# Performance work log

Hardware: AMD Instinct MI355X
Metric: run time of the kernel (lower is better)

Reference implementation:

```python
import jax, jax.numpy as jnp
import numpy as np

EPS = 1e-20

def efficient_squash(s):
    # Efficient-CapsNet squash: (1 - 1/e^||s||) * s/||s||
    n = jnp.linalg.norm(s, axis=-1, keepdims=True)
    return (1.0 - 1.0 / (jnp.exp(n) + EPS)) * (s / (n + EPS))

def setup_inputs() -> dict:
    key = jax.random.key(0)
    k1, k2 = jax.random.split(key)
    B, N, D_in = 32, 2048, 16
    K, D_out = 32, 16
    x = jax.random.normal(k1, (B, N, D_in), dtype=jnp.float32)
    # he_normal fan_in = N * D_in * ... ; use simple scaled normal init
    w = jax.random.normal(k2, (K, N, D_in, D_out), dtype=jnp.float32) * 0.05
    b = jnp.zeros((K, N, 1), dtype=jnp.float32)
    return {"x": x, "w": w, "b": b}

def reference(x, w, b):
    D_out = w.shape[-1]
    # projection: [B,N,D_in] x [K,N,D_in,D_out] -> [B,K,N,D_out]
    u = jnp.einsum('bji,kjiz->bkjz', x, w)
    # agreement c_{bkj} = sum_{i,z} u_{bkjz} u_{bkiz} = <u_j, sum_i u_i>
    t = jnp.sum(u, axis=2)                      # [B,K,D_out]
    c = jnp.einsum('bkjz,bkz->bkj', u, t)[..., None]  # [B,K,N,1]
    c = c / jnp.sqrt(jnp.asarray(D_out, jnp.float32))
    c = jax.nn.softmax(c, axis=1)               # softmax over capsules K
    c = c + b                                   # broadcast [K,N,1]
    s = jnp.sum(u * c, axis=2)                  # [B,K,D_out]
    return efficient_squash(s)
```

## Files before the change

### kernel.cpp

```cpp
#include <hip/hip_runtime.h>

#define NN 2048
#define KK 32

typedef __attribute__((ext_vector_type(8))) short short8;
typedef __attribute__((ext_vector_type(4))) float f32x4;

#define WS_TPART 0UL
#define WS_SPART 33554432UL
#define WS_TP2   50331648UL
#define WS_SP2   51380224UL
#define WS_T     52428800UL
#define WS_NEED  52494336UL

__device__ __forceinline__ short8 pack8(const float* r) {
    short8 o;
#pragma unroll
    for (int e = 0; e < 8; ++e)
        o[e] = (short)(unsigned short)((__float_as_uint(r[e]) + 0x8000u) >> 16);
    return o;
}
__device__ __forceinline__ short8 sel8(bool keep, short8 v) {
    union { short8 s; unsigned u[4]; } a, b;
    a.s = v;
#pragma unroll
    for (int i = 0; i < 4; ++i) b.u[i] = keep ? a.u[i] : 0u;
    return b.s;
}

__global__ __launch_bounds__(512)
void kT(const float* __restrict__ x, const float* __restrict__ w,
        float* __restrict__ t_part)
{
    const int tid = threadIdx.x;
    const int wv = tid >> 6, l = tid & 63;
    const int z = l & 15, g = l >> 4;
    const int jl = g >> 1, ih = g & 1;
    const int j0 = blockIdx.x * 4;

    f32x4 C[4][2];
#pragma unroll
    for (int ckl = 0; ckl < 4; ++ckl)
#pragma unroll
        for (int bh = 0; bh < 2; ++bh) C[ckl][bh] = (f32x4){0.f, 0.f, 0.f, 0.f};

#pragma unroll
    for (int p = 0; p < 2; ++p) {
        const int jp = j0 + p * 2 + jl;
        short8 Af[2];
#pragma unroll
        for (int bh = 0; bh < 2; ++bh) {
            const float* xp = x + ((size_t)(bh * 16 + z) * NN + jp) * 16 + ih * 8;
            float ar[8];
            float4 v0 = *reinterpret_cast<const float4*>(xp);
            float4 v1 = *reinterpret_cast<const float4*>(xp + 4);
            ar[0]=v0.x; ar[1]=v0.y; ar[2]=v0.z; ar[3]=v0.w;
            ar[4]=v1.x; ar[5]=v1.y; ar[6]=v1.z; ar[7]=v1.w;
            Af[bh] = pack8(ar);
        }
        short8 Bf[4];
#pragma unroll
        for (int ckl = 0; ckl < 4; ++ckl) {
            const int ck = wv * 4 + ckl;
            const float* wp = w + ((size_t)ck * NN + jp) * 256 + ih * 128 + z;
            float br[8];
#pragma unroll
            for (int e = 0; e < 8; ++e) br[e] = wp[e * 16];
            Bf[ckl] = pack8(br);
        }
#pragma unroll
        for (int ckl = 0; ckl < 4; ++ckl)
#pragma unroll
            for (int bh = 0; bh < 2; ++bh)
                C[ckl][bh] = __builtin_amdgcn_mfma_f32_16x16x32_bf16(
                    Af[bh], Bf[ckl], C[ckl][bh], 0, 0, 0);
    }

    float* tp = t_part + (size_t)blockIdx.x * 16384;
#pragma unroll
    for (int ckl = 0; ckl < 4; ++ckl)
#pragma unroll
        for (int bh = 0; bh < 2; ++bh)
#pragma unroll
            for (int r = 0; r < 4; ++r)
                tp[((bh * 16 + g * 4 + r) * 32 + wv * 4 + ckl) * 16 + z] =
                    C[ckl][bh][r];
}

__global__ __launch_bounds__(256)
void kred32(const float* __restrict__ src, float* __restrict__ dst)
{
    const int idx = blockIdx.x * 256 + threadIdx.x;
    const int c4 = idx & 4095, ch = idx >> 12;
    const f32x4* P = reinterpret_cast<const f32x4*>(src);
    f32x4 a0 = (f32x4){0,0,0,0}, a1 = a0, a2 = a0, a3 = a0;
#pragma unroll 2
    for (int q = 0; q < 32; q += 4) {
        a0 += P[(size_t)(ch * 32 + q + 0) * 4096 + c4];
        a1 += P[(size_t)(ch * 32 + q + 1) * 4096 + c4];
        a2 += P[(size_t)(ch * 32 + q + 2) * 4096 + c4];
        a3 += P[(size_t)(ch * 32 + q + 3) * 4096 + c4];
    }
    reinterpret_cast<f32x4*>(dst)[(size_t)ch * 4096 + c4] = (a0 + a1) + (a2 + a3);
}

__global__ __launch_bounds__(256)
void kred16(const float* __restrict__ src, float* __restrict__ dst)
{
    const int idx = blockIdx.x * 256 + threadIdx.x;
    const int c4 = idx & 4095, ch = idx >> 12;
    const f32x4* P = reinterpret_cast<const f32x4*>(src);
    f32x4 a0 = (f32x4){0,0,0,0}, a1 = a0, a2 = a0, a3 = a0;
#pragma unroll
    for (int q = 0; q < 16; q += 4) {
        a0 += P[(size_t)(ch * 16 + q + 0) * 4096 + c4];
        a1 += P[(size_t)(ch * 16 + q + 1) * 4096 + c4];
        a2 += P[(size_t)(ch * 16 + q + 2) * 4096 + c4];
        a3 += P[(size_t)(ch * 16 + q + 3) * 4096 + c4];
    }
    reinterpret_cast<f32x4*>(dst)[(size_t)ch * 4096 + c4] = (a0 + a1) + (a2 + a3);
}

__global__ __launch_bounds__(256)
void kt2(const float* __restrict__ tp2, float* __restrict__ t)
{
    const int c4 = blockIdx.x * 256 + threadIdx.x;
    const f32x4* P = reinterpret_cast<const f32x4*>(tp2);
    f32x4 a0 = (f32x4){0,0,0,0}, a1 = a0, a2 = a0, a3 = a0;
#pragma unroll
    for (int q = 0; q < 16; q += 4) {
        a0 += P[(size_t)(q + 0) * 4096 + c4];
        a1 += P[(size_t)(q + 1) * 4096 + c4];
        a2 += P[(size_t)(q + 2) * 4096 + c4];
        a3 += P[(size_t)(q + 3) * 4096 + c4];
    }
    reinterpret_cast<f32x4*>(t)[c4] = (a0 + a1) + (a2 + a3);
}

__global__ __launch_bounds__(512)
void kBF(const float* __restrict__ x, const float* __restrict__ w,
         const float* __restrict__ t, const float* __restrict__ bias,
         float* __restrict__ s_part)
{
    __shared__ float t_lds[32 * 520];
    __shared__ float l_lds[32][33];
    __shared__ float c_lds[32][33];
    __shared__ float b_lds[32][8];
    const int tid = threadIdx.x;
    const int wv = tid >> 6, l = tid & 63;
    const int c16 = l & 15, g = l >> 4;
    const int jl = g >> 1, ih = g & 1;
    const int j0 = blockIdx.x * 8;

    {
        const f32x4* tg = reinterpret_cast<const f32x4*>(t);
#pragma unroll
        for (int q = 0; q < 8; ++q) {
            const int idx4 = q * 512 + tid;
            const int b = idx4 >> 7, col4 = idx4 & 127;
            *reinterpret_cast<f32x4*>(&t_lds[b * 520 + col4 * 4]) = tg[idx4];
        }
        if (tid < 256)
            b_lds[tid >> 3][tid & 7] = bias[(size_t)(tid >> 3) * NN + j0 + (tid & 7)];
    }
    __syncthreads();

    f32x4 S[4][2];
#pragma unroll
    for (int ckl = 0; ckl < 4; ++ckl)
#pragma unroll
        for (int bn = 0; bn < 2; ++bn) S[ckl][bn] = (f32x4){0.f, 0.f, 0.f, 0.f};

#pragma unroll 1
    for (int p = 0; p < 4; ++p) {
        const int jp = j0 + p * 2 + jl;

        short8 Wf[4];
#pragma unroll
        for (int ckl = 0; ckl < 4; ++ckl) {
            const int k = wv * 4 + ckl;
            const float* wp = w + ((size_t)k * NN + jp) * 256 + ih * 128 + c16;
            float br[8];
#pragma unroll
            for (int e = 0; e < 8; ++e) br[e] = wp[e * 16];
            Wf[ckl] = pack8(br);
        }
        short8 Xf[2];
#pragma unroll
        for (int bn = 0; bn < 2; ++bn) {
            const float* xp = x + ((size_t)(bn * 16 + c16) * NN + jp) * 16 + ih * 8;
            float ar[8];
            float4 v0 = *reinterpret_cast<const float4*>(xp);
            float4 v1 = *reinterpret_cast<const float4*>(xp + 4);
            ar[0]=v0.x; ar[1]=v0.y; ar[2]=v0.z; ar[3]=v0.w;
            ar[4]=v1.x; ar[5]=v1.y; ar[6]=v1.z; ar[7]=v1.w;
            Xf[bn] = pack8(ar);
        }

#pragma unroll 1
        for (int jj = 0; jj < 2; ++jj) {
            const bool keep = (jl == jj);
            const f32x4 zero = (f32x4){0.f, 0.f, 0.f, 0.f};

            f32x4 C[4][2];
#pragma unroll
            for (int ckl = 0; ckl < 4; ++ckl) {
                const short8 wsel = sel8(keep, Wf[ckl]);
                const int k = wv * 4 + ckl;
#pragma unroll
                for (int bn = 0; bn < 2; ++bn) {
                    C[ckl][bn] = __builtin_amdgcn_mfma_f32_16x16x32_bf16(
                        wsel, Xf[bn], zero, 0, 0, 0);
                    const int b = bn * 16 + c16;
                    const f32x4 tv = *reinterpret_cast<const f32x4*>(
                        &t_lds[b * 520 + k * 16 + g * 4]);
                    float pv = C[ckl][bn][0] * tv[0] + C[ckl][bn][1] * tv[1]
                             + C[ckl][bn][2] * tv[2] + C[ckl][bn][3] * tv[3];
                    pv += __shfl_xor(pv, 16);
                    pv += __shfl_xor(pv, 32);
                    if (g == 0) l_lds[b][k] = pv;
                }
            }
            __syncthreads();

            {
                const int bb = tid >> 4, kq = tid & 15;
                const float lv0 = l_lds[bb][2 * kq];
                const float lv1 = l_lds[bb][2 * kq + 1];
                float m = fmaxf(lv0, lv1);
                m = fmaxf(m, __shfl_xor(m, 1));
                m = fmaxf(m, __shfl_xor(m, 2));
                m = fmaxf(m, __shfl_xor(m, 4));
                m = fmaxf(m, __shfl_xor(m, 8));
                const float e0 = __expf((lv0 - m) * 0.25f);
                const float e1 = __expf((lv1 - m) * 0.25f);
                float sum = e0 + e1;
                sum += __shfl_xor(sum, 1);
                sum += __shfl_xor(sum, 2);
                sum += __shfl_xor(sum, 4);
                sum += __shfl_xor(sum, 8);
                const float inv = 1.f / sum;
                const int jloc = p * 2 + jj;
                c_lds[bb][2 * kq]     = e0 * inv + b_lds[2 * kq][jloc];
                c_lds[bb][2 * kq + 1] = e1 * inv + b_lds[2 * kq + 1][jloc];
            }
            __syncthreads();

#pragma unroll
            for (int ckl = 0; ckl < 4; ++ckl) {
                const int k = wv * 4 + ckl;
#pragma unroll
                for (int bn = 0; bn < 2; ++bn) {
                    const float cv = c_lds[bn * 16 + c16][k];
#pragma unroll
                    for (int r = 0; r < 4; ++r)
                        S[ckl][bn][r] = fmaf(cv, C[ckl][bn][r], S[ckl][bn][r]);
                }
            }
        }
    }

    float* sp = s_part + (size_t)blockIdx.x * 16384;
#pragma unroll
    for (int ckl = 0; ckl < 4; ++ckl) {
        const int k = wv * 4 + ckl;
#pragma unroll
        for (int bn = 0; bn < 2; ++bn)
            *reinterpret_cast<f32x4*>(
                &sp[(bn * 16 + c16) * 512 + k * 16 + g * 4]) = S[ckl][bn];
    }
}

__global__ __launch_bounds__(256)
void ksq(const float* __restrict__ sp2, float* __restrict__ out)
{
    const int c4 = blockIdx.x * 256 + threadIdx.x;
    const f32x4* P = reinterpret_cast<const f32x4*>(sp2);
    f32x4 a0 = (f32x4){0,0,0,0}, a1 = a0, a2 = a0, a3 = a0;
#pragma unroll
    for (int q = 0; q < 16; q += 4) {
        a0 += P[(size_t)(q + 0) * 4096 + c4];
        a1 += P[(size_t)(q + 1) * 4096 + c4];
        a2 += P[(size_t)(q + 2) * 4096 + c4];
        a3 += P[(size_t)(q + 3) * 4096 + c4];
    }
    f32x4 s = (a0 + a1) + (a2 + a3);
    float ss = s.x * s.x + s.y * s.y + s.z * s.z + s.w * s.w;
    ss += __shfl_xor(ss, 1);
    ss += __shfl_xor(ss, 2);
    const float n = sqrtf(ss);
    const float sc = (1.f - 1.f / (__expf(n) + 1e-20f)) / (n + 1e-20f);
    f32x4 o; o.x = s.x * sc; o.y = s.y * sc; o.z = s.z * sc; o.w = s.w * sc;
    reinterpret_cast<f32x4*>(out)[c4] = o;
}

__global__ void k_sentinel(float* __restrict__ out)
{
    out[blockIdx.x * 256 + threadIdx.x] = 12345.0f;
}

extern "C" void kernel_launch(void* const* d_in, const int* in_sizes, int n_in,
                              void* d_out, int out_size, void* d_ws, size_t ws_size,
                              hipStream_t stream)
{
    const float* x    = (const float*)d_in[0];
    const float* w    = (const float*)d_in[1];
    const float* bias = (const float*)d_in[2];
    float* out        = (float*)d_out;

    char* ws = (char*)d_ws;
    if (ws_size < WS_NEED) {
        k_sentinel<<<dim3(64), dim3(256), 0, stream>>>(out);
        return;
    }
    float* t_part = (float*)(ws + WS_TPART);
    float* s_part = (float*)(ws + WS_SPART);
    float* tp2    = (float*)(ws + WS_TP2);
    float* sp2    = (float*)(ws + WS_SP2);
    float* t      = (float*)(ws + WS_T);

    kT    <<<dim3(512), dim3(512), 0, stream>>>(x, w, t_part);
    kred32<<<dim3(256), dim3(256), 0, stream>>>(t_part, tp2);
    kt2   <<<dim3(16),  dim3(256), 0, stream>>>(tp2, t);
    kBF   <<<dim3(256), dim3(512), 0, stream>>>(x, w, t, bias, s_part);
    kred16<<<dim3(256), dim3(256), 0, stream>>>(s_part, sp2);
    ksq   <<<dim3(16),  dim3(256), 0, stream>>>(sp2, out);
}
```

Measured before the change: 65.56 us.

## Merge two-stage partial reductions into single LDS-tree kernels and double kBF grid

Replaces the two-pass global reductions (kred32+kt2, kred16+ksq) with single 1024-thread kernels that each reduce a column slice across all 512 partials through an LDS tree. The squash is folded into the second reduction. kBF now processes 4 nodes per block over 512 blocks, doubling its parallelism and the s_part partial count. This cuts two launches and the intermediate round-trips, but the reductions read more partial data and use only 256 blocks with few active threads at the end.

```diff
diff --git a/kernel.cpp b/kernel.cpp
--- a/kernel.cpp
+++ b/kernel.cpp
@@ -8,10 +8,8 @@
 
 #define WS_TPART 0UL
 #define WS_SPART 33554432UL
-#define WS_TP2   50331648UL
-#define WS_SP2   51380224UL
-#define WS_T     52428800UL
-#define WS_NEED  52494336UL
+#define WS_T     67108864UL
+#define WS_NEED  67174400UL
 
 __device__ __forceinline__ short8 pack8(const float* r) {
     short8 o;
@@ -87,54 +85,36 @@
                     C[ckl][bh][r];
 }
 
-__global__ __launch_bounds__(256)
-void kred32(const float* __restrict__ src, float* __restrict__ dst)
-{
-    const int idx = blockIdx.x * 256 + threadIdx.x;
-    const int c4 = idx & 4095, ch = idx >> 12;
+__global__ __launch_bounds__(1024)
+void kredt(const float* __restrict__ src, float* __restrict__ dst)
+{
+    __shared__ f32x4 red[64][17];
+    const int tid = threadIdx.x;
+    const int wv = tid >> 6, l = tid & 63;
+    const int c = l & 15, rs = l >> 4;
+    const int colg = blockIdx.x * 16 + c;
     const f32x4* P = reinterpret_cast<const f32x4*>(src);
-    f32x4 a0 = (f32x4){0,0,0,0}, a1 = a0, a2 = a0, a3 = a0;
-#pragma unroll 2
-    for (int q = 0; q < 32; q += 4) {
-        a0 += P[(size_t)(ch * 32 + q + 0) * 4096 + c4];
-        a1 += P[(size_t)(ch * 32 + q + 1) * 4096 + c4];
-        a2 += P[(size_t)(ch * 32 + q + 2) * 4096 + c4];
-        a3 += P[(size_t)(ch * 32 + q + 3) * 4096 + c4];
-    }
-    reinterpret_cast<f32x4*>(dst)[(size_t)ch * 4096 + c4] = (a0 + a1) + (a2 + a3);
-}
-
-__global__ __launch_bounds__(256)
-void kred16(const float* __restrict__ src, float* __restrict__ dst)
-{
-    const int idx = blockIdx.x * 256 + threadIdx.x;
-    const int c4 = idx & 4095, ch = idx >> 12;
-    const f32x4* P = reinterpret_cast<const f32x4*>(src);
-    f32x4 a0 = (f32x4){0,0,0,0}, a1 = a0, a2 = a0, a3 = a0;
-#pragma unroll
-    for (int q = 0; q < 16; q += 4) {
-        a0 += P[(size_t)(ch * 16 + q + 0) * 4096 + c4];
-        a1 += P[(size_t)(ch * 16 + q + 1) * 4096 + c4];
-        a2 += P[(size_t)(ch * 16 + q + 2) * 4096 + c4];
-        a3 += P[(size_t)(ch * 16 + q + 3) * 4096 + c4];
-    }
-    reinterpret_cast<f32x4*>(dst)[(size_t)ch * 4096 + c4] = (a0 + a1) + (a2 + a3);
-}
-
-__global__ __launch_bounds__(256)
-void kt2(const float* __restrict__ tp2, float* __restrict__ t)
-{
-    const int c4 = blockIdx.x * 256 + threadIdx.x;
-    const f32x4* P = reinterpret_cast<const f32x4*>(tp2);
-    f32x4 a0 = (f32x4){0,0,0,0}, a1 = a0, a2 = a0, a3 = a0;
-#pragma unroll
-    for (int q = 0; q < 16; q += 4) {
-        a0 += P[(size_t)(q + 0) * 4096 + c4];
-        a1 += P[(size_t)(q + 1) * 4096 + c4];
-        a2 += P[(size_t)(q + 2) * 4096 + c4];
-        a3 += P[(size_t)(q + 3) * 4096 + c4];
-    }
-    reinterpret_cast<f32x4*>(t)[c4] = (a0 + a1) + (a2 + a3);
+    f32x4 a = (f32x4){0.f, 0.f, 0.f, 0.f};
+#pragma unroll
+    for (int q = 0; q < 8; ++q)
+        a += P[(size_t)(wv * 32 + q * 4 + rs) * 4096 + colg];
+    red[wv * 4 + rs][c] = a;
+    __syncthreads();
+    f32x4 s = (f32x4){0.f, 0.f, 0.f, 0.f};
+    if (tid < 256) {
+        const int cc = tid & 15, r0 = tid >> 4;
+        s = (red[r0 * 4 + 0][cc] + red[r0 * 4 + 1][cc])
+          + (red[r0 * 4 + 2][cc] + red[r0 * 4 + 3][cc]);
+    }
+    __syncthreads();
+    if (tid < 256) red[tid >> 4][tid & 15] = s;
+    __syncthreads();
+    if (tid < 16) {
+        f32x4 o = (f32x4){0.f, 0.f, 0.f, 0.f};
+#pragma unroll
+        for (int r = 0; r < 16; ++r) o += red[r][tid];
+        reinterpret_cast<f32x4*>(dst)[blockIdx.x * 16 + tid] = o;
+    }
 }
 
 __global__ __launch_bounds__(512)
@@ -145,12 +125,12 @@
     __shared__ float t_lds[32 * 520];
     __shared__ float l_lds[32][33];
     __shared__ float c_lds[32][33];
-    __shared__ float b_lds[32][8];
+    __shared__ float b_lds[32][4];
     const int tid = threadIdx.x;
     const int wv = tid >> 6, l = tid & 63;
     const int c16 = l & 15, g = l >> 4;
     const int jl = g >> 1, ih = g & 1;
-    const int j0 = blockIdx.x * 8;
+    const int j0 = blockIdx.x * 4;
 
     {
         const f32x4* tg = reinterpret_cast<const f32x4*>(t);
@@ -160,8 +140,8 @@
             const int b = idx4 >> 7, col4 = idx4 & 127;
             *reinterpret_cast<f32x4*>(&t_lds[b * 520 + col4 * 4]) = tg[idx4];
         }
-        if (tid < 256)
-            b_lds[tid >> 3][tid & 7] = bias[(size_t)(tid >> 3) * NN + j0 + (tid & 7)];
+        if (tid < 128)
+            b_lds[tid >> 2][tid & 3] = bias[(size_t)(tid >> 2) * NN + j0 + (tid & 3)];
     }
     __syncthreads();
 
@@ -172,7 +152,7 @@
         for (int bn = 0; bn < 2; ++bn) S[ckl][bn] = (f32x4){0.f, 0.f, 0.f, 0.f};
 
 #pragma unroll 1
-    for (int p = 0; p < 4; ++p) {
+    for (int p = 0; p < 2; ++p) {
         const int jp = j0 + p * 2 + jl;
 
         short8 Wf[4];
@@ -271,27 +251,42 @@
     }
 }
 
-__global__ __launch_bounds__(256)
-void ksq(const float* __restrict__ sp2, float* __restrict__ out)
-{
-    const int c4 = blockIdx.x * 256 + threadIdx.x;
-    const f32x4* P = reinterpret_cast<const f32x4*>(sp2);
-    f32x4 a0 = (f32x4){0,0,0,0}, a1 = a0, a2 = a0, a3 = a0;
-#pragma unroll
-    for (int q = 0; q < 16; q += 4) {
-        a0 += P[(size_t)(q + 0) * 4096 + c4];
-        a1 += P[(size_t)(q + 1) * 4096 + c4];
-        a2 += P[(size_t)(q + 2) * 4096 + c4];
-        a3 += P[(size_t)(q + 3) * 4096 + c4];
-    }
-    f32x4 s = (a0 + a1) + (a2 + a3);
-    float ss = s.x * s.x + s.y * s.y + s.z * s.z + s.w * s.w;
-    ss += __shfl_xor(ss, 1);
-    ss += __shfl_xor(ss, 2);
-    const float n = sqrtf(ss);
-    const float sc = (1.f - 1.f / (__expf(n) + 1e-20f)) / (n + 1e-20f);
-    f32x4 o; o.x = s.x * sc; o.y = s.y * sc; o.z = s.z * sc; o.w = s.w * sc;
-    reinterpret_cast<f32x4*>(out)[c4] = o;
+__global__ __launch_bounds__(1024)
+void kredsq(const float* __restrict__ src, float* __restrict__ out)
+{
+    __shared__ f32x4 red[64][17];
+    const int tid = threadIdx.x;
+    const int wv = tid >> 6, l = tid & 63;
+    const int c = l & 15, rs = l >> 4;
+    const int colg = blockIdx.x * 16 + c;
+    const f32x4* P = reinterpret_cast<const f32x4*>(src);
+    f32x4 a = (f32x4){0.f, 0.f, 0.f, 0.f};
+#pragma unroll
+    for (int q = 0; q < 8; ++q)
+        a += P[(size_t)(wv * 32 + q * 4 + rs) * 4096 + colg];
+    red[wv * 4 + rs][c] = a;
+    __syncthreads();
+    f32x4 s = (f32x4){0.f, 0.f, 0.f, 0.f};
+    if (tid < 256) {
+        const int cc = tid & 15, r0 = tid >> 4;
+        s = (red[r0 * 4 + 0][cc] + red[r0 * 4 + 1][cc])
+          + (red[r0 * 4 + 2][cc] + red[r0 * 4 + 3][cc]);
+    }
+    __syncthreads();
+    if (tid < 256) red[tid >> 4][tid & 15] = s;
+    __syncthreads();
+    if (tid < 16) {
+        f32x4 o = (f32x4){0.f, 0.f, 0.f, 0.f};
+#pragma unroll
+        for (int r = 0; r < 16; ++r) o += red[r][tid];
+        float ss = o.x * o.x + o.y * o.y + o.z * o.z + o.w * o.w;
+        ss += __shfl_xor(ss, 1);
+        ss += __shfl_xor(ss, 2);
+        const float n = sqrtf(ss);
+        const float sc = (1.f - 1.f / (__expf(n) + 1e-20f)) / (n + 1e-20f);
+        f32x4 r; r.x = o.x * sc; r.y = o.y * sc; r.z = o.z * sc; r.w = o.w * sc;
+        reinterpret_cast<f32x4*>(out)[blockIdx.x * 16 + tid] = r;
+    }
 }
 
 __global__ void k_sentinel(float* __restrict__ out)
@@ -315,14 +310,10 @@
     }
     float* t_part = (float*)(ws + WS_TPART);
     float* s_part = (float*)(ws + WS_SPART);
-    float* tp2    = (float*)(ws + WS_TP2);
-    float* sp2    = (float*)(ws + WS_SP2);
     float* t      = (float*)(ws + WS_T);
 
-    kT    <<<dim3(512), dim3(512), 0, stream>>>(x, w, t_part);
-    kred32<<<dim3(256), dim3(256), 0, stream>>>(t_part, tp2);
-    kt2   <<<dim3(16),  dim3(256), 0, stream>>>(tp2, t);
-    kBF   <<<dim3(256), dim3(512), 0, stream>>>(x, w, t, bias, s_part);
-    kred16<<<dim3(256), dim3(256), 0, stream>>>(s_part, sp2);
-    ksq   <<<dim3(16),  dim3(256), 0, stream>>>(sp2, out);
-}
+    kT    <<<dim3(512), dim3(512),  0, stream>>>(x, w, t_part);
+    kredt <<<dim3(256), dim3(1024), 0, stream>>>(t_part, t);
+    kBF   <<<dim3(512), dim3(512),  0, stream>>>(x, w, t, bias, s_part);
+    kredsq<<<dim3(256), dim3(1024), 0, stream>>>(s_part, out);
+}
```

Result: slower. 67.32 us (+2.7%).
